# Kernel optimization log

Measured on AMD Instinct MI355X. Metric: run time of the kernel, lower is better.

## Reference

```python
import jax, jax.numpy as jnp
import numpy as np

BATCH = 4096
DIM = 512
TEMP = 0.1

def setup_inputs() -> dict:
    key = jax.random.key(0)
    k1, k2 = jax.random.split(key)
    emb_i = jax.random.normal(k1, (BATCH, DIM), dtype=jnp.float32)
    emb_j = jax.random.normal(k2, (BATCH, DIM), dtype=jnp.float32)
    return {"emb_i": emb_i, "emb_j": emb_j}

def _l2_normalize(x, eps=1e-12):
    # matches torch F.normalize(dim=1): x / max(||x||, eps)
    norm = jnp.sqrt(jnp.sum(x * x, axis=1, keepdims=True))
    return x / jnp.maximum(norm, eps)

def reference(emb_i, emb_j):
    n = emb_i.shape[0]
    z_i = _l2_normalize(emb_i)
    z_j = _l2_normalize(emb_j)
    reps = jnp.concatenate([z_i, z_j], axis=0)  # [2N, D], rows unit-norm
    # cosine similarity of unit vectors == dot product -> GEMM instead of O(N^2 D) broadcast
    sim = reps @ reps.T  # [2N, 2N]
    # positives: diag offsets +N and -N
    pos_ij = jnp.sum(z_i * z_j, axis=1)  # diag(sim, +N)
    pos_ji = pos_ij                      # diag(sim, -N) is identical by symmetry
    positives = jnp.concatenate([pos_ij, pos_ji], axis=0)  # [2N]
    nominator = jnp.exp(positives / TEMP)
    neg_mask = 1.0 - jnp.eye(2 * n, dtype=sim.dtype)
    denominator = jnp.sum(neg_mask * jnp.exp(sim / TEMP), axis=1)  # [2N]
    loss_partial = -jnp.log(nominator / denominator)
    return jnp.sum(loss_partial) / (2 * n)
```

## Files before the change

### kernel.cpp

```cpp
#include <hip/hip_runtime.h>
#include <hip/hip_bf16.h>
#include <math.h>

#define N_ROWS 4096
#define DIM    512
#define M_ROWS 8192
#define BK     32
#define NTILE  64
#define NB     2080
#define NSTEP  16
#define EXP_SCALE 14.4269504088896340736f

typedef unsigned short ushort_t;
typedef __attribute__((ext_vector_type(8))) short short8;
typedef __attribute__((ext_vector_type(4))) float f32x4;

__device__ __forceinline__ ushort_t f2bf(float x) {
  unsigned int bits = __float_as_uint(x);
  unsigned int lsb = (bits >> 16) & 1u;
  bits += 0x7fffu + lsb;
  return (ushort_t)(bits >> 16);
}

__device__ __forceinline__ void store4bf(ushort_t* p, float4 v, float s) {
  union { ushort_t u[4]; uint2 d; } pk;
  pk.u[0] = f2bf(v.x * s);
  pk.u[1] = f2bf(v.y * s);
  pk.u[2] = f2bf(v.z * s);
  pk.u[3] = f2bf(v.w * s);
  *(uint2*)p = pk.d;
}

__device__ __forceinline__ void async16(const ushort_t* g, ushort_t* l) {
  __builtin_amdgcn_global_load_lds(
      (const __attribute__((address_space(1))) void*)g,
      (__attribute__((address_space(3))) void*)l,
      16, 0, 0);
}

__global__ __launch_bounds__(256) void norm_kernel(
    const float* __restrict__ ei, const float* __restrict__ ej,
    ushort_t* __restrict__ reps, float* __restrict__ pos,
    float* __restrict__ denom) {
  int wave = threadIdx.x >> 6;
  int lane = threadIdx.x & 63;
  int b = blockIdx.x * 4 + wave;
  if (lane == 0) {
    denom[b] = 0.0f;
    denom[b + N_ROWS] = 0.0f;
  }
  const float4* pi = (const float4*)(ei + (size_t)b * DIM);
  const float4* pj = (const float4*)(ej + (size_t)b * DIM);
  float4 a0 = pi[lane];
  float4 a1 = pi[lane + 64];
  float4 b0 = pj[lane];
  float4 b1 = pj[lane + 64];

  float si = a0.x*a0.x + a0.y*a0.y + a0.z*a0.z + a0.w*a0.w
           + a1.x*a1.x + a1.y*a1.y + a1.z*a1.z + a1.w*a1.w;
  float sj = b0.x*b0.x + b0.y*b0.y + b0.z*b0.z + b0.w*b0.w
           + b1.x*b1.x + b1.y*b1.y + b1.z*b1.z + b1.w*b1.w;
  float dp = a0.x*b0.x + a0.y*b0.y + a0.z*b0.z + a0.w*b0.w
           + a1.x*b1.x + a1.y*b1.y + a1.z*b1.z + a1.w*b1.w;

#pragma unroll
  for (int m = 32; m >= 1; m >>= 1) {
    si += __shfl_xor(si, m, 64);
    sj += __shfl_xor(sj, m, 64);
    dp += __shfl_xor(dp, m, 64);
  }
  float ii = 1.0f / fmaxf(sqrtf(si), 1e-12f);
  float ij = 1.0f / fmaxf(sqrtf(sj), 1e-12f);
  if (lane == 0) pos[b] = dp * ii * ij;

  ushort_t* ri = reps + (size_t)b * DIM;
  ushort_t* rj = reps + (size_t)(b + N_ROWS) * DIM;
  store4bf(ri + lane * 4,       a0, ii);
  store4bf(ri + 256 + lane * 4, a1, ii);
  store4bf(rj + lane * 4,       b0, ij);
  store4bf(rj + 256 + lane * 4, b1, ij);
}

__global__ __launch_bounds__(256) void sim_kernel(
    const ushort_t* __restrict__ reps, float* __restrict__ denom) {
  int id = blockIdx.x;
  id = (id & 7) * (NB / 8) + (id >> 3);

  int bi, bj;
  {
    int rem = id, Si = 0, Sj = 0, fnd = 0;
    for (int s_j = 0; s_j < 4 && !fnd; ++s_j)
      for (int s_i = 0; s_i <= s_j && !fnd; ++s_i) {
        int sz = (s_i == s_j) ? 136 : 256;
        if (rem < sz) { Si = s_i; Sj = s_j; fnd = 1; }
        else rem -= sz;
      }
    if (Si == Sj) {
      int tj = 0;
      while ((tj + 1) * (tj + 2) / 2 <= rem) ++tj;
      int ti = rem - tj * (tj + 1) / 2;
      bi = Si * 16 + ti;
      bj = Sj * 16 + tj;
    } else {
      bi = Si * 16 + (rem & 15);
      bj = Sj * 16 + (rem >> 4);
    }
  }

  __shared__ ushort_t As[2][128 * BK];
  __shared__ ushort_t Bs[2][128 * BK];

  int tid  = threadIdx.x;
  int wave = tid >> 6, lane = tid & 63;
  int wr = wave >> 1, wc = wave & 1;
  int quad = lane >> 4, l15 = lane & 15;

  int c0 = wave * 2, c1 = c0 + 1;
  int srow  = lane >> 2;
  int selem = ((lane & 3) ^ ((srow >> 1) & 3)) * 8;
  const ushort_t* gA0 = reps + (size_t)(bi * 128 + c0 * 16 + srow) * DIM + selem;
  const ushort_t* gA1 = reps + (size_t)(bi * 128 + c1 * 16 + srow) * DIM + selem;
  const ushort_t* gB0 = reps + (size_t)(bj * 128 + c0 * 16 + srow) * DIM + selem;
  const ushort_t* gB1 = reps + (size_t)(bj * 128 + c1 * 16 + srow) * DIM + selem;

#define STAGE(D, KOFF) do {                         \
    async16(gA0 + (KOFF), &As[D][c0 * 512]);        \
    async16(gA1 + (KOFF), &As[D][c1 * 512]);        \
    async16(gB0 + (KOFF), &Bs[D][c0 * 512]);        \
    async16(gB1 + (KOFF), &Bs[D][c1 * 512]);        \
  } while (0)

  int sqr = (quad ^ ((l15 >> 1) & 3)) * 8;

  f32x4 zero4 = {0.0f, 0.0f, 0.0f, 0.0f};
  f32x4 acc[4][4];
#pragma unroll
  for (int tr = 0; tr < 4; ++tr)
#pragma unroll
    for (int tc = 0; tc < 4; ++tc) acc[tr][tc] = zero4;

  STAGE(0, 0);

  for (int kk = 0; kk < NSTEP; ++kk) {
    int cur = kk & 1;
    int nk = ((kk + 1) & 15) * BK;

    STAGE(cur ^ 1, nk);
    asm volatile("s_waitcnt vmcnt(4)" ::: "memory");
    __builtin_amdgcn_s_barrier();

    short8 aF[4], bF[4];
#pragma unroll
    for (int t = 0; t < 4; ++t) {
      aF[t] = *(const short8*)(&As[cur][(wr * 64 + t * 16 + l15) * BK + sqr]);
      bF[t] = *(const short8*)(&Bs[cur][(wc * 64 + t * 16 + l15) * BK + sqr]);
    }
    __builtin_amdgcn_s_setprio(1);
#pragma unroll
    for (int tr = 0; tr < 4; ++tr)
#pragma unroll
      for (int tc = 0; tc < 4; ++tc)
        acc[tr][tc] = __builtin_amdgcn_mfma_f32_16x16x32_bf16(
            aF[tr], bF[tc], acc[tr][tc], 0, 0, 0);
    __builtin_amdgcn_s_setprio(0);
    __builtin_amdgcn_s_barrier();
  }
  asm volatile("s_waitcnt vmcnt(0)" ::: "memory");

  int rowg_base = bi * 128 + wr * 64;
  int colg_base = bj * 128 + wc * 64;

  f32x4 rsum[4];
  float csum[4] = {0.0f, 0.0f, 0.0f, 0.0f};
#pragma unroll
  for (int tr = 0; tr < 4; ++tr) rsum[tr] = zero4;

#pragma unroll
  for (int tr = 0; tr < 4; ++tr) {
    int rowg0 = rowg_base + tr * 16 + quad * 4;
#pragma unroll
    for (int tc = 0; tc < 4; ++tc) {
      int colg = colg_base + tc * 16 + l15;
      f32x4 a = acc[tr][tc];
      f32x4 e;
#pragma unroll
      for (int r = 0; r < 4; ++r) {
        float v = exp2f(a[r] * EXP_SCALE);
        e[r] = ((rowg0 + r) == colg) ? 0.0f : v;
      }
      rsum[tr] += e;
      csum[tc] += e[0] + e[1] + e[2] + e[3];
    }
  }

#pragma unroll
  for (int m = 1; m <= 8; m <<= 1)
#pragma unroll
    for (int tr = 0; tr < 4; ++tr)
#pragma unroll
      for (int r = 0; r < 4; ++r)
        rsum[tr][r] += __shfl_xor(rsum[tr][r], m, 64);

  if (l15 == 0) {
#pragma unroll
    for (int tr = 0; tr < 4; ++tr)
#pragma unroll
      for (int r = 0; r < 4; ++r)
        atomicAdd(&denom[rowg_base + tr * 16 + quad * 4 + r], rsum[tr][r]);
  }

  if (bi != bj) {
#pragma unroll
    for (int m = 16; m <= 32; m <<= 1)
#pragma unroll
      for (int tc = 0; tc < 4; ++tc)
        csum[tc] += __shfl_xor(csum[tc], m, 64);
    if (quad == 0) {
#pragma unroll
      for (int tc = 0; tc < 4; ++tc)
        atomicAdd(&denom[colg_base + tc * 16 + l15], csum[tc]);
    }
  }
}

__global__ __launch_bounds__(1024) void loss_kernel(
    const float* __restrict__ denom, const float* __restrict__ pos,
    float* __restrict__ out) {
  __shared__ float red[16];
  int tid = threadIdx.x;
  float p = 0.0f;
  for (int r = tid; r < M_ROWS; r += 1024)
    p += logf(denom[r]) - pos[r & (N_ROWS - 1)] * 10.0f;
#pragma unroll
  for (int m = 32; m >= 1; m >>= 1) p += __shfl_xor(p, m, 64);
  if ((tid & 63) == 0) red[tid >> 6] = p;
  __syncthreads();
  if (tid == 0) {
    float s = 0.0f;
#pragma unroll
    for (int i = 0; i < 16; ++i) s += red[i];
    out[0] = s * (1.0f / M_ROWS);
  }
}

extern "C" void kernel_launch(void* const* d_in, const int* in_sizes, int n_in,
                              void* d_out, int out_size, void* d_ws, size_t ws_size,
                              hipStream_t stream) {
  const float* ei = (const float*)d_in[0];
  const float* ej = (const float*)d_in[1];
  float* out = (float*)d_out;

  char* ws = (char*)d_ws;
  ushort_t* reps = (ushort_t*)ws;
  float* denom = (float*)(ws + (size_t)M_ROWS * DIM * 2);
  float* pos = (float*)(ws + (size_t)M_ROWS * DIM * 2 + M_ROWS * 4);

  norm_kernel<<<N_ROWS / 4, 256, 0, stream>>>(ei, ej, reps, pos, denom);
  sim_kernel<<<NB, 256, 0, stream>>>(reps, denom);
  loss_kernel<<<1, 1024, 0, stream>>>(denom, pos, out);
}
```

Before: 136.2 us.

## Load MFMA operands directly from global memory into registers, dropping LDS staging

Removes the shared-memory double buffer fed by async global-to-LDS loads, along with the block barriers. Each wave now loads its bf16 A/B fragments straight from global memory into registers, using a two-deep register ping-pong across the fully unrolled K loop. The aim is to cut LDS traffic and barrier stalls. The cost is that operand reuse across waves now depends on cache instead of LDS, so global/L2 load traffic roughly doubles and register pressure rises.

```diff
diff --git a/kernel.cpp b/kernel.cpp
--- a/kernel.cpp
+++ b/kernel.cpp
@@ -29,13 +29,6 @@
   pk.u[2] = f2bf(v.z * s);
   pk.u[3] = f2bf(v.w * s);
   *(uint2*)p = pk.d;
-}
-
-__device__ __forceinline__ void async16(const ushort_t* g, ushort_t* l) {
-  __builtin_amdgcn_global_load_lds(
-      (const __attribute__((address_space(1))) void*)g,
-      (__attribute__((address_space(3))) void*)l,
-      16, 0, 0);
 }
 
 __global__ __launch_bounds__(256) void norm_kernel(
@@ -107,30 +100,18 @@
     }
   }
 
-  __shared__ ushort_t As[2][128 * BK];
-  __shared__ ushort_t Bs[2][128 * BK];
-
   int tid  = threadIdx.x;
   int wave = tid >> 6, lane = tid & 63;
   int wr = wave >> 1, wc = wave & 1;
   int quad = lane >> 4, l15 = lane & 15;
 
-  int c0 = wave * 2, c1 = c0 + 1;
-  int srow  = lane >> 2;
-  int selem = ((lane & 3) ^ ((srow >> 1) & 3)) * 8;
-  const ushort_t* gA0 = reps + (size_t)(bi * 128 + c0 * 16 + srow) * DIM + selem;
-  const ushort_t* gA1 = reps + (size_t)(bi * 128 + c1 * 16 + srow) * DIM + selem;
-  const ushort_t* gB0 = reps + (size_t)(bj * 128 + c0 * 16 + srow) * DIM + selem;
-  const ushort_t* gB1 = reps + (size_t)(bj * 128 + c1 * 16 + srow) * DIM + selem;
-
-#define STAGE(D, KOFF) do {                         \
-    async16(gA0 + (KOFF), &As[D][c0 * 512]);        \
-    async16(gA1 + (KOFF), &As[D][c1 * 512]);        \
-    async16(gB0 + (KOFF), &Bs[D][c0 * 512]);        \
-    async16(gB1 + (KOFF), &Bs[D][c1 * 512]);        \
-  } while (0)
-
-  int sqr = (quad ^ ((l15 >> 1) & 3)) * 8;
+  const ushort_t* pA[4];
+  const ushort_t* pB[4];
+#pragma unroll
+  for (int t = 0; t < 4; ++t) {
+    pA[t] = reps + (size_t)(bi * 128 + wr * 64 + t * 16 + l15) * DIM + quad * 8;
+    pB[t] = reps + (size_t)(bj * 128 + wc * 64 + t * 16 + l15) * DIM + quad * 8;
+  }
 
   f32x4 zero4 = {0.0f, 0.0f, 0.0f, 0.0f};
   f32x4 acc[4][4];
@@ -139,33 +120,37 @@
 #pragma unroll
     for (int tc = 0; tc < 4; ++tc) acc[tr][tc] = zero4;
 
-  STAGE(0, 0);
-
-  for (int kk = 0; kk < NSTEP; ++kk) {
-    int cur = kk & 1;
-    int nk = ((kk + 1) & 15) * BK;
-
-    STAGE(cur ^ 1, nk);
-    asm volatile("s_waitcnt vmcnt(4)" ::: "memory");
-    __builtin_amdgcn_s_barrier();
-
-    short8 aF[4], bF[4];
-#pragma unroll
-    for (int t = 0; t < 4; ++t) {
-      aF[t] = *(const short8*)(&As[cur][(wr * 64 + t * 16 + l15) * BK + sqr]);
-      bF[t] = *(const short8*)(&Bs[cur][(wc * 64 + t * 16 + l15) * BK + sqr]);
-    }
-    __builtin_amdgcn_s_setprio(1);
-#pragma unroll
-    for (int tr = 0; tr < 4; ++tr)
-#pragma unroll
-      for (int tc = 0; tc < 4; ++tc)
-        acc[tr][tc] = __builtin_amdgcn_mfma_f32_16x16x32_bf16(
-            aF[tr], bF[tc], acc[tr][tc], 0, 0, 0);
-    __builtin_amdgcn_s_setprio(0);
-    __builtin_amdgcn_s_barrier();
-  }
-  asm volatile("s_waitcnt vmcnt(0)" ::: "memory");
+#define LOADF(DST, PTRS, KOFF) do {                          \
+    DST[0] = *(const short8*)(PTRS[0] + (KOFF));             \
+    DST[1] = *(const short8*)(PTRS[1] + (KOFF));             \
+    DST[2] = *(const short8*)(PTRS[2] + (KOFF));             \
+    DST[3] = *(const short8*)(PTRS[3] + (KOFF));             \
+  } while (0)
+
+#define MFMA16(AF, BF) do {                                                \
+    _Pragma("unroll")                                                      \
+    for (int tr = 0; tr < 4; ++tr)                                         \
+      _Pragma("unroll")                                                    \
+      for (int tc = 0; tc < 4; ++tc)                                       \
+        acc[tr][tc] = __builtin_amdgcn_mfma_f32_16x16x32_bf16(             \
+            AF[tr], BF[tc], acc[tr][tc], 0, 0, 0);                         \
+  } while (0)
+
+  short8 aX[4], bX[4], aY[4], bY[4];
+  LOADF(aX, pA, 0);
+  LOADF(bX, pB, 0);
+
+#pragma unroll
+  for (int kk = 0; kk < NSTEP; kk += 2) {
+    LOADF(aY, pA, (kk + 1) * BK);
+    LOADF(bY, pB, (kk + 1) * BK);
+    MFMA16(aX, bX);
+    if (kk + 2 < NSTEP) {
+      LOADF(aX, pA, (kk + 2) * BK);
+      LOADF(bX, pB, (kk + 2) * BK);
+    }
+    MFMA16(aY, bY);
+  }
 
   int rowg_base = bi * 128 + wr * 64;
   int colg_base = bj * 128 + wc * 64;
```

After: 236.5 us. +73.6%, slower.

## Switch similarity GEMM to FP8 MFMA and fuse loss reduction into last block

Applied to the files above, without the earlier changes.

Normalized embeddings are now quantized to FP8 e4m3 instead of bf16, and the similarity GEMM uses the fp8 16x16x32 MFMA. This halves operand bytes and doubles the K covered per staged tile, so there are fewer k-steps. The separate loss kernel is removed: a global atomic counter lets the last finishing sim block compute the log-sum reduction, saving one launch. FP8 loses mantissa precision, and because the exp uses a 1/0.1 temperature scale, that error may push the loss past tolerance.

```diff
diff --git a/kernel.cpp b/kernel.cpp
--- a/kernel.cpp
+++ b/kernel.cpp
@@ -5,33 +5,48 @@
 #define N_ROWS 4096
 #define DIM    512
 #define M_ROWS 8192
-#define BK     32
-#define NTILE  64
 #define NB     2080
-#define NSTEP  16
+#define NSTEP  8
 #define EXP_SCALE 14.4269504088896340736f
 
-typedef unsigned short ushort_t;
-typedef __attribute__((ext_vector_type(8))) short short8;
+typedef unsigned char u8;
+typedef unsigned long long u64;
 typedef __attribute__((ext_vector_type(4))) float f32x4;
 
-__device__ __forceinline__ ushort_t f2bf(float x) {
-  unsigned int bits = __float_as_uint(x);
-  unsigned int lsb = (bits >> 16) & 1u;
-  bits += 0x7fffu + lsb;
-  return (ushort_t)(bits >> 16);
-}
-
-__device__ __forceinline__ void store4bf(ushort_t* p, float4 v, float s) {
-  union { ushort_t u[4]; uint2 d; } pk;
-  pk.u[0] = f2bf(v.x * s);
-  pk.u[1] = f2bf(v.y * s);
-  pk.u[2] = f2bf(v.z * s);
-  pk.u[3] = f2bf(v.w * s);
-  *(uint2*)p = pk.d;
-}
-
-__device__ __forceinline__ void async16(const ushort_t* g, ushort_t* l) {
+__device__ __forceinline__ unsigned int f2e4m3(float x) {
+  unsigned int b = __float_as_uint(x);
+  unsigned int s = (b >> 24) & 0x80u;
+  int e = (int)((b >> 23) & 0xffu);
+  unsigned int m = b & 0x7fffffu;
+  int ne = e - 127 + 7;
+  unsigned int out;
+  if (ne >= 1) {
+    unsigned int q = ((unsigned int)ne << 3) | (m >> 20);
+    unsigned int rem = m & 0xfffffu;
+    unsigned int rnd = (rem > 0x80000u) || ((rem == 0x80000u) && (q & 1u));
+    out = q + rnd;
+  } else {
+    int sh = 21 - ne;
+    if (sh > 24) {
+      out = 0;
+    } else {
+      unsigned int full = 0x800000u | m;
+      unsigned int q = full >> sh;
+      unsigned int rem = full & ((1u << sh) - 1u);
+      unsigned int half = 1u << (sh - 1);
+      unsigned int rnd = (rem > half) || ((rem == half) && (q & 1u));
+      out = q + rnd;
+    }
+  }
+  return s | out;
+}
+
+__device__ __forceinline__ unsigned int pack4fp8(float4 v, float s) {
+  return f2e4m3(v.x * s) | (f2e4m3(v.y * s) << 8) |
+         (f2e4m3(v.z * s) << 16) | (f2e4m3(v.w * s) << 24);
+}
+
+__device__ __forceinline__ void async16(const u8* g, u8* l) {
   __builtin_amdgcn_global_load_lds(
       (const __attribute__((address_space(1))) void*)g,
       (__attribute__((address_space(3))) void*)l,
@@ -40,11 +55,12 @@
 
 __global__ __launch_bounds__(256) void norm_kernel(
     const float* __restrict__ ei, const float* __restrict__ ej,
-    ushort_t* __restrict__ reps, float* __restrict__ pos,
-    float* __restrict__ denom) {
+    u8* __restrict__ reps, float* __restrict__ pos,
+    float* __restrict__ denom, unsigned int* __restrict__ ctr) {
   int wave = threadIdx.x >> 6;
   int lane = threadIdx.x & 63;
   int b = blockIdx.x * 4 + wave;
+  if (blockIdx.x == 0 && threadIdx.x == 0) *ctr = 0u;
   if (lane == 0) {
     denom[b] = 0.0f;
     denom[b + N_ROWS] = 0.0f;
@@ -73,16 +89,18 @@
   float ij = 1.0f / fmaxf(sqrtf(sj), 1e-12f);
   if (lane == 0) pos[b] = dp * ii * ij;
 
-  ushort_t* ri = reps + (size_t)b * DIM;
-  ushort_t* rj = reps + (size_t)(b + N_ROWS) * DIM;
-  store4bf(ri + lane * 4,       a0, ii);
-  store4bf(ri + 256 + lane * 4, a1, ii);
-  store4bf(rj + lane * 4,       b0, ij);
-  store4bf(rj + 256 + lane * 4, b1, ij);
+  unsigned int* ri = (unsigned int*)(reps + (size_t)b * DIM);
+  unsigned int* rj = (unsigned int*)(reps + (size_t)(b + N_ROWS) * DIM);
+  ri[lane]      = pack4fp8(a0, ii);
+  ri[lane + 64] = pack4fp8(a1, ii);
+  rj[lane]      = pack4fp8(b0, ij);
+  rj[lane + 64] = pack4fp8(b1, ij);
 }
 
 __global__ __launch_bounds__(256) void sim_kernel(
-    const ushort_t* __restrict__ reps, float* __restrict__ denom) {
+    const u8* __restrict__ reps, float* __restrict__ denom,
+    const float* __restrict__ pos, float* __restrict__ out,
+    unsigned int* __restrict__ ctr) {
   int id = blockIdx.x;
   id = (id & 7) * (NB / 8) + (id >> 3);
 
@@ -107,8 +125,10 @@
     }
   }
 
-  __shared__ ushort_t As[2][128 * BK];
-  __shared__ ushort_t Bs[2][128 * BK];
+  __shared__ u8 As[2][8192];
+  __shared__ u8 Bs[2][8192];
+  __shared__ float red[4];
+  __shared__ int lastflag;
 
   int tid  = threadIdx.x;
   int wave = tid >> 6, lane = tid & 63;
@@ -116,21 +136,26 @@
   int quad = lane >> 4, l15 = lane & 15;
 
   int c0 = wave * 2, c1 = c0 + 1;
-  int srow  = lane >> 2;
-  int selem = ((lane & 3) ^ ((srow >> 1) & 3)) * 8;
-  const ushort_t* gA0 = reps + (size_t)(bi * 128 + c0 * 16 + srow) * DIM + selem;
-  const ushort_t* gA1 = reps + (size_t)(bi * 128 + c1 * 16 + srow) * DIM + selem;
-  const ushort_t* gB0 = reps + (size_t)(bj * 128 + c0 * 16 + srow) * DIM + selem;
-  const ushort_t* gB1 = reps + (size_t)(bj * 128 + c1 * 16 + srow) * DIM + selem;
-
-#define STAGE(D, KOFF) do {                         \
-    async16(gA0 + (KOFF), &As[D][c0 * 512]);        \
-    async16(gA1 + (KOFF), &As[D][c1 * 512]);        \
-    async16(gB0 + (KOFF), &Bs[D][c0 * 512]);        \
-    async16(gB1 + (KOFF), &Bs[D][c1 * 512]);        \
+  int srow = lane >> 2;
+  int scol = ((lane & 3) ^ (srow & 3)) * 16;
+  const u8* gA0 = reps + (size_t)(bi * 128 + c0 * 16 + srow) * DIM + scol;
+  const u8* gA1 = reps + (size_t)(bi * 128 + c1 * 16 + srow) * DIM + scol;
+  const u8* gB0 = reps + (size_t)(bj * 128 + c0 * 16 + srow) * DIM + scol;
+  const u8* gB1 = reps + (size_t)(bj * 128 + c1 * 16 + srow) * DIM + scol;
+
+#define STAGE(D, KC) do {                              \
+    int o_ = (KC) * 64;                                \
+    async16(gA0 + o_, &As[D][c0 * 1024]);              \
+    async16(gA1 + o_, &As[D][c1 * 1024]);              \
+    async16(gB0 + o_, &Bs[D][c0 * 1024]);              \
+    async16(gB1 + o_, &Bs[D][c1 * 1024]);              \
   } while (0)
 
-  int sqr = (quad ^ ((l15 >> 1) & 3)) * 8;
+  int qh = quad >> 1, ql = quad & 1, x2 = l15 & 3;
+  int sw0 = ((qh ^ x2) * 16) + ql * 8;
+  int sw1 = (((2 + qh) ^ x2) * 16) + ql * 8;
+  int abase = (wr * 64 + l15) * 64;
+  int bbase = (wc * 64 + l15) * 64;
 
   f32x4 zero4 = {0.0f, 0.0f, 0.0f, 0.0f};
   f32x4 acc[4][4];
@@ -143,25 +168,31 @@
 
   for (int kk = 0; kk < NSTEP; ++kk) {
     int cur = kk & 1;
-    int nk = ((kk + 1) & 15) * BK;
-
-    STAGE(cur ^ 1, nk);
+    int nc = (kk + 1) & 7;
+
+    STAGE(cur ^ 1, nc);
     asm volatile("s_waitcnt vmcnt(4)" ::: "memory");
     __builtin_amdgcn_s_barrier();
 
-    short8 aF[4], bF[4];
+    const u8* Ah = &As[cur][0];
+    const u8* Bh = &Bs[cur][0];
+    long aF[4][2], bF[4][2];
 #pragma unroll
     for (int t = 0; t < 4; ++t) {
-      aF[t] = *(const short8*)(&As[cur][(wr * 64 + t * 16 + l15) * BK + sqr]);
-      bF[t] = *(const short8*)(&Bs[cur][(wc * 64 + t * 16 + l15) * BK + sqr]);
+      aF[t][0] = *(const long*)(Ah + abase + t * 1024 + sw0);
+      aF[t][1] = *(const long*)(Ah + abase + t * 1024 + sw1);
+      bF[t][0] = *(const long*)(Bh + bbase + t * 1024 + sw0);
+      bF[t][1] = *(const long*)(Bh + bbase + t * 1024 + sw1);
     }
     __builtin_amdgcn_s_setprio(1);
 #pragma unroll
-    for (int tr = 0; tr < 4; ++tr)
-#pragma unroll
-      for (int tc = 0; tc < 4; ++tc)
-        acc[tr][tc] = __builtin_amdgcn_mfma_f32_16x16x32_bf16(
-            aF[tr], bF[tc], acc[tr][tc], 0, 0, 0);
+    for (int ks = 0; ks < 2; ++ks)
+#pragma unroll
+      for (int tr = 0; tr < 4; ++tr)
+#pragma unroll
+        for (int tc = 0; tc < 4; ++tc)
+          acc[tr][tc] = __builtin_amdgcn_mfma_f32_16x16x32_fp8_fp8(
+              aF[tr][ks], bF[tc][ks], acc[tr][tc], 0, 0, 0);
     __builtin_amdgcn_s_setprio(0);
     __builtin_amdgcn_s_barrier();
   }
@@ -221,25 +252,21 @@
         atomicAdd(&denom[colg_base + tc * 16 + l15], csum[tc]);
     }
   }
-}
-
-__global__ __launch_bounds__(1024) void loss_kernel(
-    const float* __restrict__ denom, const float* __restrict__ pos,
-    float* __restrict__ out) {
-  __shared__ float red[16];
-  int tid = threadIdx.x;
-  float p = 0.0f;
-  for (int r = tid; r < M_ROWS; r += 1024)
-    p += logf(denom[r]) - pos[r & (N_ROWS - 1)] * 10.0f;
-#pragma unroll
-  for (int m = 32; m >= 1; m >>= 1) p += __shfl_xor(p, m, 64);
-  if ((tid & 63) == 0) red[tid >> 6] = p;
+
+  __threadfence();
+  if (tid == 0) lastflag = (atomicAdd(ctr, 1u) == (unsigned int)(NB - 1));
   __syncthreads();
-  if (tid == 0) {
-    float s = 0.0f;
-#pragma unroll
-    for (int i = 0; i < 16; ++i) s += red[i];
-    out[0] = s * (1.0f / M_ROWS);
+  if (lastflag) {
+    __threadfence();
+    float p = 0.0f;
+    for (int r = tid; r < M_ROWS; r += 256)
+      p += logf(denom[r]) - pos[r & (N_ROWS - 1)] * 10.0f;
+#pragma unroll
+    for (int m = 32; m >= 1; m >>= 1) p += __shfl_xor(p, m, 64);
+    if ((tid & 63) == 0) red[tid >> 6] = p;
+    __syncthreads();
+    if (tid == 0)
+      out[0] = (red[0] + red[1] + red[2] + red[3]) * (1.0f / M_ROWS);
   }
 }
 
@@ -251,11 +278,11 @@
   float* out = (float*)d_out;
 
   char* ws = (char*)d_ws;
-  ushort_t* reps = (ushort_t*)ws;
-  float* denom = (float*)(ws + (size_t)M_ROWS * DIM * 2);
-  float* pos = (float*)(ws + (size_t)M_ROWS * DIM * 2 + M_ROWS * 4);
-
-  norm_kernel<<<N_ROWS / 4, 256, 0, stream>>>(ei, ej, reps, pos, denom);
-  sim_kernel<<<NB, 256, 0, stream>>>(reps, denom);
-  loss_kernel<<<1, 1024, 0, stream>>>(denom, pos, out);
-}
+  u8* reps = (u8*)ws;
+  float* denom = (float*)(ws + (size_t)4 * 1024 * 1024);
+  float* pos = (float*)(ws + (size_t)4 * 1024 * 1024 + 32768);
+  unsigned int* ctr = (unsigned int*)(ws + (size_t)4 * 1024 * 1024 + 32768 + 16384);
+
+  norm_kernel<<<N_ROWS / 4, 256, 0, stream>>>(ei, ej, reps, pos, denom, ctr);
+  sim_kernel<<<NB, 256, 0, stream>>>(reps, denom, pos, out, ctr);
+}
```

After: 245.7 us. +80.4%, slower.
